# Kernel optimization log

Measured on AMD Instinct MI355X. Metric: run time of the kernel, lower is better.

Reference implementation:

```python
import jax, jax.numpy as jnp
import numpy as np
import math

Z_DIM = 1024
DOWN = 512
UP = 1024
HEADS = 16
ROPE_HD = 64
HEAD_DIM = Z_DIM // HEADS  # 64, used only in softmax scale
V_HD = UP // HEADS


def _rope(x, num_heads, head_dim, base=10000.0):
    # x: [bs, L, num_heads*head_dim] -> [bs, num_heads, L, head_dim]
    bs, L, _ = x.shape
    theta = 1.0 / (base ** (jnp.arange(0, head_dim, 2, dtype=jnp.float32) / head_dim))
    pe = jnp.arange(L, dtype=jnp.float32)[:, None] * theta[None, :]  # [L, hd/2]
    # NOTE: faithful to source, which stores sin(pos) in cos_pos and cos(pos) in sin_pos
    cos_pos = jnp.repeat(jnp.sin(pe), 2, axis=-1)  # [L, hd]
    sin_pos = jnp.repeat(jnp.cos(pe), 2, axis=-1)
    q = x.reshape(bs, L, num_heads, head_dim).transpose(0, 2, 1, 3)
    q2 = jnp.stack([-q[..., 1::2], q[..., ::2]], axis=-1).reshape(q.shape)
    return q * cos_pos + q2 * sin_pos


def setup_inputs() -> dict:
    key = jax.random.key(0)
    ks = jax.random.split(key, 20)
    B, S = 2, 2048
    s = lambda fan_in: 1.0 / math.sqrt(fan_in)
    d = {
        'query': jax.random.normal(ks[0], (B, S, Z_DIM), jnp.float32),
        'key': jax.random.normal(ks[1], (B, S, Z_DIM), jnp.float32),
        'value': jax.random.normal(ks[2], (B, S, Z_DIM), jnp.float32),
        'w_dkv': jax.random.uniform(ks[3], (Z_DIM, DOWN), jnp.float32, -s(Z_DIM), s(Z_DIM)),
        'b_dkv': jnp.zeros((DOWN,), jnp.float32),
        'w_uk': jax.random.uniform(ks[4], (DOWN, UP), jnp.float32, -s(DOWN), s(DOWN)),
        'b_uk': jnp.zeros((UP,), jnp.float32),
        'w_uv': jax.random.uniform(ks[5], (DOWN, UP), jnp.float32, -s(DOWN), s(DOWN)),
        'b_uv': jnp.zeros((UP,), jnp.float32),
        'w_dq': jax.random.uniform(ks[6], (Z_DIM, DOWN), jnp.float32, -s(Z_DIM), s(Z_DIM)),
        'b_dq': jnp.zeros((DOWN,), jnp.float32),
        'w_uq': jax.random.uniform(ks[7], (DOWN, UP), jnp.float32, -s(DOWN), s(DOWN)),
        'b_uq': jnp.zeros((UP,), jnp.float32),
        'w_qr': jax.random.uniform(ks[8], (DOWN, ROPE_HD * HEADS), jnp.float32, -s(DOWN), s(DOWN)),
        'b_qr': jnp.zeros((ROPE_HD * HEADS,), jnp.float32),
        'w_kr': jax.random.uniform(ks[9], (Z_DIM, ROPE_HD), jnp.float32, -s(Z_DIM), s(Z_DIM)),
        'b_kr': jnp.zeros((ROPE_HD,), jnp.float32),
        'w_fc': jax.random.uniform(ks[10], (HEADS * V_HD, Z_DIM), jnp.float32, -s(HEADS * V_HD), s(HEADS * V_HD)),
        'b_fc': jnp.zeros((Z_DIM,), jnp.float32),
    }
    return d


def reference(query, key, value, w_dkv, b_dkv, w_uk, b_uk, w_uv, b_uv,
              w_dq, b_dq, w_uq, b_uq, w_qr, b_qr, w_kr, b_kr, w_fc, b_fc):
    bs, S, _ = query.shape
    c_t_kv = key @ w_dkv + b_dkv                      # [B,S,down]
    k_t_c = c_t_kv @ w_uk + b_uk                      # [B,S,up]
    v_t_c = c_t_kv @ w_uv + b_uv                      # [B,S,up]
    c_t_q = query @ w_dq + b_dq                       # [B,S,down]
    q_t_c = c_t_q @ w_uq + b_uq                       # [B,S,up]
    q_t_r = _rope(c_t_q @ w_qr + b_qr, HEADS, ROPE_HD)  # [B,H,S,rope_hd]
    k_t_r = _rope(key @ w_kr + b_kr, 1, ROPE_HD)         # [B,1,S,rope_hd]

    q_t_c = q_t_c.reshape(bs, S, HEADS, V_HD).transpose(0, 2, 1, 3)  # [B,H,S,dc]
    q = jnp.concatenate([q_t_c, q_t_r], axis=-1)                      # [B,H,S,dc+dr]
    k_t_c = k_t_c.reshape(bs, S, HEADS, V_HD).transpose(0, 2, 1, 3)
    k = jnp.concatenate([k_t_c, jnp.broadcast_to(k_t_r, (bs, HEADS, S, ROPE_HD))], axis=-1)

    scores = jnp.einsum('bhqd,bhkd->bhqk', q, k)
    scale = math.sqrt(HEAD_DIM) + math.sqrt(ROPE_HD)
    attn = jax.nn.softmax(scores / scale, axis=-1)    # dropout is identity (eval / p=0)

    v = v_t_c.reshape(bs, S, HEADS, V_HD).transpose(0, 2, 1, 3)
    out = jnp.einsum('bhqk,bhkd->bhqd', attn, v)      # [B,H,S,v_hd]
    out = out.transpose(0, 2, 1, 3).reshape(bs, S, HEADS * V_HD)
    return out @ w_fc + b_fc
```

## Files before the change

### kernel.cpp

```cpp
#include <hip/hip_runtime.h>
#include <hip/hip_bf16.h>
#include <hip/hip_fp16.h>

typedef __attribute__((ext_vector_type(8))) short    bf16x8;
typedef __attribute__((ext_vector_type(4))) float    f32x4;
typedef __attribute__((ext_vector_type(4))) _Float16 f16x4;
typedef __attribute__((ext_vector_type(8))) _Float16 f16x8;
typedef __attribute__((ext_vector_type(2))) __fp16   fp16x2_raw;

typedef const void __attribute__((address_space(1))) gvoid_t;
typedef void __attribute__((address_space(3)))       lvoid_t;

static __device__ __forceinline__ void gload_lds16(const void* g, void* l) {
    __builtin_amdgcn_global_load_lds((gvoid_t*)g, (lvoid_t*)l, 16, 0, 0);
}

static __device__ __forceinline__ short bfbits(float f) {
    union { __hip_bfloat16 h; short s; } u;
    u.h = __float2bfloat16(f);
    return u.s;
}

__global__ __launch_bounds__(256) void cvt_bf16_dual(const float* __restrict__ q,
                                                     const float* __restrict__ k,
                                                     __hip_bfloat16* __restrict__ qd,
                                                     __hip_bfloat16* __restrict__ kd, int n8) {
    int t = blockIdx.x * 256 + threadIdx.x;
    const float* src;
    __hip_bfloat16* dst;
    int i;
    if (t < n8)          { src = q; dst = qd; i = t; }
    else if (t < 2 * n8) { src = k; dst = kd; i = t - n8; }
    else return;
    float4 a = ((const float4*)src)[2 * i];
    float4 b = ((const float4*)src)[2 * i + 1];
    bf16x8 o;
    o[0] = bfbits(a.x); o[1] = bfbits(a.y); o[2] = bfbits(a.z); o[3] = bfbits(a.w);
    o[4] = bfbits(b.x); o[5] = bfbits(b.y); o[6] = bfbits(b.z); o[7] = bfbits(b.w);
    ((bf16x8*)dst)[i] = o;
}

struct TJob { const float* src; __hip_bfloat16* dst; int K, N, tx; };
struct TJobPack { TJob j[8]; int start[8]; };

__global__ __launch_bounds__(256) void transpose_cvt_batch(TJobPack P) {
    __shared__ __hip_bfloat16 tile[64][72];
    const int bid = blockIdx.x;
    int ji = 0;
#pragma unroll
    for (int k = 1; k < 8; ++k) if (bid >= P.start[k]) ji = k;
    const TJob J = P.j[ji];
    const int local = bid - P.start[ji];
    const int kb = (local % J.tx) * 64;
    const int nb = (local / J.tx) * 64;
    const int c  = threadIdx.x & 63;
    const int r0 = threadIdx.x >> 6;
    if (nb < J.N) {
#pragma unroll
        for (int i = 0; i < 16; ++i) {
            int r = r0 + i * 4;
            tile[r][c] = __float2bfloat16(J.src[(size_t)(kb + r) * J.N + nb + c]);
        }
        __syncthreads();
#pragma unroll
        for (int i = 0; i < 16; ++i) {
            int r = r0 + i * 4;
            J.dst[(size_t)(nb + r) * J.K + kb + c] = tile[c][r];
        }
    } else {
        __hip_bfloat16 z = __float2bfloat16(0.0f);
#pragma unroll
        for (int i = 0; i < 16; ++i) {
            int r = r0 + i * 4;
            J.dst[(size_t)(nb + r) * J.K + kb + c] = z;
        }
    }
}

__global__ __launch_bounds__(256) void bias_prep(const float* __restrict__ b_dkv, const float* __restrict__ b_kr,
                                                 const float* __restrict__ b_uk,  const float* __restrict__ b_uv,
                                                 const float* __restrict__ b_uq,  const float* __restrict__ b_qr,
                                                 float* __restrict__ bcat1, float* __restrict__ bcat2,
                                                 float* __restrict__ bcat3) {
    int t = blockIdx.x * 256 + threadIdx.x;
    if (t < 640) {
        bcat1[t] = (t < 512) ? b_dkv[t] : ((t - 512) < 64 ? b_kr[t - 512] : 0.0f);
    } else if (t < 2688) {
        int u = t - 640;
        bcat2[u] = (u < 1024) ? b_uq[u] : b_qr[u - 1024];
    } else if (t < 4736) {
        int u = t - 2688;
        bcat3[u] = (u < 1024) ? b_uk[u] : b_uv[u - 1024];
    }
}

struct GJob {
    const __hip_bfloat16* A; const __hip_bfloat16* Bt; const float* bias;
    void* C0; void* C1; int N, K, lda, ldb, ldc; float scale; int mode;
};

__global__ __launch_bounds__(256) void gemm_dual(GJob j0, GJob j1, int split) {
    __shared__ __align__(16) __hip_bfloat16 sA[2][64 * 32];
    __shared__ __align__(16) __hip_bfloat16 sB[2][128 * 32];
    const GJob J  = (blockIdx.x < (unsigned)split) ? j0 : j1;
    const int bx  = (blockIdx.x < (unsigned)split) ? blockIdx.x : blockIdx.x - split;
    const int tid  = threadIdx.x;
    const int wid  = tid >> 6;
    const int lane = tid & 63;
    const int lr   = lane & 15;
    const int lg   = lane >> 4;
    const int mb   = blockIdx.y * 64;
    const int nb   = bx * 128;
    const int wr   = (wid >> 1) * 32;
    const int wc   = (wid & 1) * 64;

    auto stage = [&](int bufi, int k0) {
        {
            int e   = wid * 512 + lane * 8;
            int row = e >> 5, col = e & 31;
            gload_lds16(J.A + (size_t)(mb + row) * J.lda + (k0 + col), &sA[bufi][wid * 512]);
        }
#pragma unroll
        for (int j = 0; j < 2; ++j) {
            int cb  = wid * 2 + j;
            int e   = cb * 512 + lane * 8;
            int row = e >> 5, col = e & 31;
            gload_lds16(J.Bt + (size_t)(nb + row) * J.ldb + (k0 + col), &sB[bufi][cb * 512]);
        }
    };

    f32x4 acc[2][4] = {};
    const int nt = J.K / 32;
    stage(0, 0);
    asm volatile("s_waitcnt vmcnt(0)" ::: "memory");
    __syncthreads();

    for (int t = 0; t < nt; ++t) {
        const int cur = t & 1;
        if (t + 1 < nt) stage(cur ^ 1, (t + 1) * 32);
        bf16x8 af[2], bfr[4];
#pragma unroll
        for (int m = 0; m < 2; ++m)
            af[m] = *(const bf16x8*)&sA[cur][(wr + m * 16 + lr) * 32 + lg * 8];
#pragma unroll
        for (int n = 0; n < 4; ++n)
            bfr[n] = *(const bf16x8*)&sB[cur][(wc + n * 16 + lr) * 32 + lg * 8];
#pragma unroll
        for (int m = 0; m < 2; ++m)
#pragma unroll
            for (int n = 0; n < 4; ++n)
                acc[m][n] = __builtin_amdgcn_mfma_f32_16x16x32_bf16(af[m], bfr[n], acc[m][n], 0, 0, 0);
        asm volatile("s_waitcnt vmcnt(0)" ::: "memory");
        __syncthreads();
    }

#pragma unroll
    for (int n = 0; n < 4; ++n) {
        int col  = nb + wc + n * 16 + lr;
        float bv = J.bias ? J.bias[col] : 0.0f;
#pragma unroll
        for (int m = 0; m < 2; ++m) {
#pragma unroll
            for (int r = 0; r < 4; ++r) {
                int row    = mb + wr + m * 16 + lg * 4 + r;
                float val  = (acc[m][n][r] + bv) * J.scale;
                if (J.mode == 1) ((float*)J.C0)[(size_t)row * J.ldc + col] = val;
                else             ((__hip_bfloat16*)J.C0)[(size_t)row * J.ldc + col] = __float2bfloat16(val);
            }
        }
    }
}

__global__ __launch_bounds__(256) void gemm128_dual(GJob j0, GJob j1, int split, int Rtot) {
    __shared__ __align__(16) char smem[128 * 132 * 2];
    __hip_bfloat16* sA = (__hip_bfloat16*)smem;
    __hip_bfloat16* sB = (__hip_bfloat16*)(smem + 16384);
    const GJob J  = (blockIdx.x < (unsigned)split) ? j0 : j1;
    const int bx  = (blockIdx.x < (unsigned)split) ? blockIdx.x : blockIdx.x - split;
    const int tid  = threadIdx.x;
    const int wid  = tid >> 6;
    const int lane = tid & 63;
    const int lr   = lane & 15;
    const int lg   = lane >> 4;
    const int mb   = blockIdx.y * 128;
    const int nb   = bx * 128;
    const int wr   = (wid >> 1) * 64;
    const int wc   = (wid & 1) * 64;

    auto stage = [&](int bufi, int k0) {
#pragma unroll
        for (int j = 0; j < 2; ++j) {
            int c   = wid * 2 + j;
            int e   = c * 512 + lane * 8;
            int row = e >> 5, col = e & 31;
            gload_lds16(J.A + (size_t)(mb + row) * J.lda + (k0 + col), &sA[bufi * 4096 + c * 512]);
        }
#pragma unroll
        for (int j = 0; j < 2; ++j) {
            int c   = wid * 2 + j;
            int e   = c * 512 + lane * 8;
            int row = e >> 5, col = e & 31;
            gload_lds16(J.Bt + (size_t)(nb + row) * J.ldb + (k0 + col), &sB[bufi * 4096 + c * 512]);
        }
    };

    f32x4 acc[4][4] = {};
    const int nt = J.K / 32;
    stage(0, 0);
    asm volatile("s_waitcnt vmcnt(0)" ::: "memory");
    __syncthreads();

    for (int t = 0; t < nt; ++t) {
        const int cur = t & 1;
        if (t + 1 < nt) stage(cur ^ 1, (t + 1) * 32);
        bf16x8 af[4], bfr[4];
#pragma unroll
        for (int m = 0; m < 4; ++m)
            af[m] = *(const bf16x8*)&sA[cur * 4096 + (wr + m * 16 + lr) * 32 + lg * 8];
#pragma unroll
        for (int n = 0; n < 4; ++n)
            bfr[n] = *(const bf16x8*)&sB[cur * 4096 + (wc + n * 16 + lr) * 32 + lg * 8];
#pragma unroll
        for (int m = 0; m < 4; ++m)
#pragma unroll
            for (int n = 0; n < 4; ++n)
                acc[m][n] = __builtin_amdgcn_mfma_f32_16x16x32_bf16(af[m], bfr[n], acc[m][n], 0, 0, 0);
        asm volatile("s_waitcnt vmcnt(0)" ::: "memory");
        __syncthreads();
    }

    if (J.mode == 3 && nb >= 1024) {
        _Float16* T = (_Float16*)smem;
#pragma unroll
        for (int n = 0; n < 4; ++n) {
            int cl = wc + n * 16 + lr;
            float bv = J.bias[nb + cl];
#pragma unroll
            for (int m = 0; m < 4; ++m)
#pragma unroll
                for (int r = 0; r < 4; ++r)
                    T[cl * 132 + wr + m * 16 + lg * 4 + r] =
                        (_Float16)((acc[m][n][r] + bv) * J.scale);
        }
        __syncthreads();
        const int vd   = tid >> 1;
        const int half = tid & 1;
        _Float16* dst = (_Float16*)J.C1 + (size_t)(nb - 1024 + vd) * Rtot + mb + half * 64;
        const _Float16* srcT = T + vd * 132 + half * 64;
#pragma unroll
        for (int j = 0; j < 8; ++j)
            *(f16x8*)&dst[j * 8] = *(const f16x8*)&srcT[j * 8];
        return;
    }

#pragma unroll
    for (int n = 0; n < 4; ++n) {
        int col  = nb + wc + n * 16 + lr;
        float bv = J.bias ? J.bias[col] : 0.0f;
#pragma unroll
        for (int m = 0; m < 4; ++m) {
#pragma unroll
            for (int r = 0; r < 4; ++r) {
                int row    = mb + wr + m * 16 + lg * 4 + r;
                float val  = (acc[m][n][r] + bv) * J.scale;
                if (J.mode == 3) ((__hip_bfloat16*)J.C0)[(size_t)row * 1024 + col] = __float2bfloat16(val);
                else             ((__hip_bfloat16*)J.C0)[(size_t)row * J.ldc + col] = __float2bfloat16(val);
            }
        }
    }
}

__global__ __launch_bounds__(256) void rope_kernel(__hip_bfloat16* __restrict__ qrope,
                                                   __hip_bfloat16* __restrict__ krope,
                                                   int R, int S) {
    int t = blockIdx.x * 256 + threadIdx.x;
    const int nq = R * 512;
    __hip_bfloat16* x;
    int i, row, rowstride, hh;
    if (t < nq)               { i = t & 31; hh = (t >> 5) & 15; row = t >> 9; x = qrope; rowstride = 2048; }
    else if (t < nq + R * 32) { t -= nq; i = t & 31; hh = 0; row = t >> 5; x = krope; rowstride = 640; }
    else return;
    int pos = row & (S - 1);
    float theta = __expf(-0.28782313662425572f * (float)i);
    float pe = (float)pos * theta;
    float sp, cp;
    __sincosf(pe, &sp, &cp);
    size_t idx = (size_t)row * rowstride + hh * 64 + 2 * i;
    float x0 = __bfloat162float(x[idx]);
    float x1 = __bfloat162float(x[idx + 1]);
    x[idx]     = __float2bfloat16(x0 * sp - x1 * cp);
    x[idx + 1] = __float2bfloat16(x1 * sp + x0 * cp);
}

__global__ __launch_bounds__(512, 4) void attn_kernel(const __hip_bfloat16* __restrict__ qcat,
                                                      const __hip_bfloat16* __restrict__ ktc,
                                                      const __hip_bfloat16* __restrict__ kr,
                                                      const _Float16* __restrict__ vtcT,
                                                      __hip_bfloat16* __restrict__ outp,
                                                      int S, int R) {
    __shared__ __align__(16) char lds[2][24 * 1024];
    const int tid  = threadIdx.x;
    const int wid  = tid >> 6;
    const int lane = tid & 63;
    const int lr   = lane & 15;
    const int lg   = lane >> 4;

    const int NQ   = S / 128;
    const int L    = blockIdx.x;
    const int slot = L >> 3;
    const int gg   = (L & 7) + 8 * (slot / NQ);
    const int qt   = slot % NQ;
    const int h    = gg & 15;
    const int b    = gg >> 4;
    const size_t base = (size_t)b * S;
    const int qb   = qt * 128 + wid * 16;

    auto stage = [&](int bufi, int kt) {
        char* bufK = lds[bufi];
        char* bufV = lds[bufi] + 16 * 1024;
#pragma unroll
        for (int j = 0; j < 2; ++j) {
            int c   = wid * 2 + j;
            int rho = c * 4 + (lane >> 4);
            int u   = (lane & 15) ^ (rho & 15);
            const __hip_bfloat16* src = (u < 8)
                ? ktc + (base + kt + rho) * 1024 + h * 64 + u * 8
                : kr  + (base + kt + rho) * 640 + (u & 7) * 8;
            gload_lds16(src, bufK + c * 1024);
        }
        {
            int c   = wid;
            int rho = c * 8 + (lane >> 3);
            int u   = (lane & 7) ^ (rho & 7);
            gload_lds16(vtcT + (size_t)(h * 64 + rho) * R + base + kt + u * 8,
                        bufV + c * 1024);
        }
    };

    bf16x8 qf[4];
    {
        size_t row = base + qb + lr;
        const __hip_bfloat16* pq = qcat + row * 2048 + h * 64;
        qf[0] = *(const bf16x8*)(pq + lg * 8);
        qf[1] = *(const bf16x8*)(pq + 32 + lg * 8);
        qf[2] = *(const bf16x8*)(pq + 1024 + lg * 8);
        qf[3] = *(const bf16x8*)(pq + 1024 + 32 + lg * 8);
    }

    int kbase[4], vbase[4];
#pragma unroll
    for (int c = 0; c < 4; ++c)
        kbase[c] = lr * 256 + (((c * 4 + lg) ^ lr) << 4);
#pragma unroll
    for (int st = 0; st < 4; ++st)
        vbase[st] = lr * 128 + ((((st * 2 + (lg >> 1)) ^ (lr & 7)) << 4) + (lg & 1) * 8);

    f32x4 oacc[4] = {};
    float lrun = 0.0f;

    const int NT = S / 64;
    stage(0, 0);
    __syncthreads();

    for (int t = 0; t < NT; ++t) {
        const int cur = t & 1;
        if (t + 1 < NT) stage(cur ^ 1, (t + 1) * 64);

        const char* bufK = lds[cur];
        const char* bufV = lds[cur] + 16 * 1024;

        f32x4 sacc[4] = {};
        __builtin_amdgcn_s_setprio(1);
#pragma unroll
        for (int st = 0; st < 4; ++st)
#pragma unroll
            for (int c = 0; c < 4; ++c) {
                bf16x8 kf = *(const bf16x8*)(bufK + st * 4096 + kbase[c]);
                sacc[st] = __builtin_amdgcn_mfma_f32_16x16x32_bf16(kf, qf[c], sacc[st], 0, 0, 0);
            }
        __builtin_amdgcn_s_setprio(0);

        float p[4][4];
#pragma unroll
        for (int st = 0; st < 4; ++st)
#pragma unroll
            for (int r = 0; r < 4; ++r) {
                p[st][r] = __builtin_exp2f(sacc[st][r]);
                lrun += p[st][r];
            }
        __builtin_amdgcn_s_setprio(1);
#pragma unroll
        for (int st = 0; st < 4; ++st) {
            union { fp16x2_raw h2[2]; f16x4 v; } pu;
            pu.h2[0] = __builtin_amdgcn_cvt_pkrtz(p[st][0], p[st][1]);
            pu.h2[1] = __builtin_amdgcn_cvt_pkrtz(p[st][2], p[st][3]);
#pragma unroll
            for (int vt = 0; vt < 4; ++vt) {
                f16x4 vf = *(const f16x4*)(bufV + vt * 2048 + vbase[st]);
                oacc[vt] = __builtin_amdgcn_mfma_f32_16x16x16f16(vf, pu.v, oacc[vt], 0, 0, 0);
            }
        }
        __builtin_amdgcn_s_setprio(0);
        __syncthreads();
    }

    lrun += __shfl_xor(lrun, 16);
    lrun += __shfl_xor(lrun, 32);
    float inv = 1.0f / lrun;
    size_t rowoff = (base + qb + lr) << 10;
#pragma unroll
    for (int vt = 0; vt < 4; ++vt)
#pragma unroll
        for (int r = 0; r < 4; ++r)
            outp[rowoff + h * 64 + vt * 16 + lg * 4 + r] =
                __float2bfloat16(oacc[vt][r] * inv);
}

extern "C" void kernel_launch(void* const* d_in, const int* in_sizes, int n_in,
                              void* d_out, int out_size, void* d_ws, size_t ws_size,
                              hipStream_t stream) {
    const float* query = (const float*)d_in[0];
    const float* key   = (const float*)d_in[1];
    const float* w_dkv = (const float*)d_in[3];
    const float* b_dkv = (const float*)d_in[4];
    const float* w_uk  = (const float*)d_in[5];
    const float* b_uk  = (const float*)d_in[6];
    const float* w_uv  = (const float*)d_in[7];
    const float* b_uv  = (const float*)d_in[8];
    const float* w_dq  = (const float*)d_in[9];
    const float* b_dq  = (const float*)d_in[10];
    const float* w_uq  = (const float*)d_in[11];
    const float* b_uq  = (const float*)d_in[12];
    const float* w_qr  = (const float*)d_in[13];
    const float* b_qr  = (const float*)d_in[14];
    const float* w_kr  = (const float*)d_in[15];
    const float* b_kr  = (const float*)d_in[16];
    const float* w_fc  = (const float*)d_in[17];
    const float* b_fc  = (const float*)d_in[18];

    const int B = 2;
    const int R = in_sizes[0] / 1024;
    const int S = R / B;
    const float QSCALE = 1.4426950408889634f / 16.0f;

    char* ws = (char*)d_ws;
    size_t off = 0;
    auto alloc = [&](size_t bytes) -> char* {
        char* p = ws + off;
        off += (bytes + 255) & ~(size_t)255;
        return p;
    };

    __hip_bfloat16* q_bf  = (__hip_bfloat16*)alloc((size_t)R * 1024 * 2);
    __hip_bfloat16* k_bf  = (__hip_bfloat16*)alloc((size_t)R * 1024 * 2);
    __hip_bfloat16* wcat1 = (__hip_bfloat16*)alloc(640 * 1024 * 2);
    __hip_bfloat16* wdq_t = (__hip_bfloat16*)alloc(512 * 1024 * 2);
    __hip_bfloat16* wcat3 = (__hip_bfloat16*)alloc(2048 * 512 * 2);
    __hip_bfloat16* wcat2 = (__hip_bfloat16*)alloc(2048 * 512 * 2);
    __hip_bfloat16* wfc_t = (__hip_bfloat16*)alloc(1024 * 1024 * 2);
    float*          bcat1 = (float*)alloc(640 * 4);
    float*          bcat2 = (float*)alloc(2048 * 4);
    float*          bcat3 = (float*)alloc(2048 * 4);
    __hip_bfloat16* ckkr  = (__hip_bfloat16*)alloc((size_t)R * 640 * 2);
    __hip_bfloat16* c_q   = (__hip_bfloat16*)alloc((size_t)R * 512 * 2);
    __hip_bfloat16* ktc   = (__hip_bfloat16*)alloc((size_t)R * 1024 * 2);
    _Float16*       vtcT  = (_Float16*)alloc((size_t)R * 1024 * 2);
    __hip_bfloat16* qcat  = (__hip_bfloat16*)alloc((size_t)R * 2048 * 2);
    __hip_bfloat16* attn_out = q_bf;

    cvt_bf16_dual<<<dim3(2 * R * 1024 / 8 / 256), 256, 0, stream>>>(query, key, q_bf, k_bf, R * 1024 / 8);

    TJobPack P;
    P.j[0] = {w_dkv, wcat1,              1024, 512,  16};
    P.j[1] = {w_kr,  wcat1 + 512 * 1024, 1024, 64,   16};
    P.j[2] = {w_dq,  wdq_t,              1024, 512,  16};
    P.j[3] = {w_uk,  wcat3,              512,  1024, 8};
    P.j[4] = {w_uv,  wcat3 + 1024 * 512, 512,  1024, 8};
    P.j[5] = {w_uq,  wcat2,              512,  1024, 8};
    P.j[6] = {w_qr,  wcat2 + 1024 * 512, 512,  1024, 8};
    P.j[7] = {w_fc,  wfc_t,              1024, 1024, 16};
    int st = 0;
    const int counts[8] = {128, 32, 128, 128, 128, 128, 128, 256};
    for (int i = 0; i < 8; ++i) { P.start[i] = st; st += counts[i]; }
    transpose_cvt_batch<<<dim3(st), 256, 0, stream>>>(P);

    bias_prep<<<dim3(19), 256, 0, stream>>>(b_dkv, b_kr, b_uk, b_uv, b_uq, b_qr, bcat1, bcat2, bcat3);

    GJob ja0 = {k_bf, wcat1, bcat1, ckkr, nullptr, 640, 1024, 1024, 1024, 640, 1.0f, 0};
    GJob ja1 = {q_bf, wdq_t, b_dq,  c_q,  nullptr, 512, 1024, 1024, 1024, 512, 1.0f, 0};
    gemm_dual<<<dim3(9, R / 64), 256, 0, stream>>>(ja0, ja1, 5);

    GJob jb0 = {ckkr, wcat3, bcat3, ktc,  vtcT,    2048, 512, 640, 512, 1024, 1.0f,   3};
    GJob jb1 = {c_q,  wcat2, bcat2, qcat, nullptr, 2048, 512, 512, 512, 2048, QSCALE, 0};
    gemm128_dual<<<dim3(32, R / 128), 256, 0, stream>>>(jb0, jb1, 16, R);

    rope_kernel<<<dim3((R * 512 + R * 32 + 255) / 256), 256, 0, stream>>>(qcat + 1024, ckkr + 512, R, S);

    attn_kernel<<<dim3((S / 128) * 16 * B), 512, 0, stream>>>(qcat, ktc, ckkr + 512, vtcT, attn_out, S, R);

    GJob jc0 = {attn_out, wfc_t, b_fc, d_out, nullptr, 1024, 1024, 1024, 1024, 1024, 1.0f, 1};
    gemm_dual<<<dim3(8, R / 64), 256, 0, stream>>>(jc0, jc0, 8);
}
```

Before: 179.6 us.

## Fuse RoPE into GEMM epilogues, merge prep kernels, use fdot2 for softmax sum

Merges the bf16 conversion, weight transpose and bias concatenation kernels into a single prep launch. Applies the rotary embedding directly in the GEMM epilogues via lane shuffles, removing the separate rope kernel and its read-modify-write pass. Replaces the scalar softmax denominator accumulation with fp16 dot2 on the packed probabilities. This adds sincos work and shuffles to the epilogues, and the row sum now uses fp16-rounded values.

```diff
diff --git a/kernel.cpp b/kernel.cpp
--- a/kernel.cpp
+++ b/kernel.cpp
@@ -21,76 +21,84 @@
     return u.s;
 }
 
-__global__ __launch_bounds__(256) void cvt_bf16_dual(const float* __restrict__ q,
-                                                     const float* __restrict__ k,
-                                                     __hip_bfloat16* __restrict__ qd,
-                                                     __hip_bfloat16* __restrict__ kd, int n8) {
-    int t = blockIdx.x * 256 + threadIdx.x;
-    const float* src;
-    __hip_bfloat16* dst;
-    int i;
-    if (t < n8)          { src = q; dst = qd; i = t; }
-    else if (t < 2 * n8) { src = k; dst = kd; i = t - n8; }
-    else return;
-    float4 a = ((const float4*)src)[2 * i];
-    float4 b = ((const float4*)src)[2 * i + 1];
-    bf16x8 o;
-    o[0] = bfbits(a.x); o[1] = bfbits(a.y); o[2] = bfbits(a.z); o[3] = bfbits(a.w);
-    o[4] = bfbits(b.x); o[5] = bfbits(b.y); o[6] = bfbits(b.z); o[7] = bfbits(b.w);
-    ((bf16x8*)dst)[i] = o;
+static __device__ __forceinline__ float rope_val(float val, int col, int row, int Smask) {
+    float other = __shfl_xor(val, 1);
+    float theta = __expf(-0.28782313662425572f * (float)((col >> 1) & 31));
+    float sp, cp;
+    __sincosf((float)(row & Smask) * theta, &sp, &cp);
+    return (col & 1) ? fmaf(val, sp, other * cp) : fmaf(val, sp, -other * cp);
 }
 
 struct TJob { const float* src; __hip_bfloat16* dst; int K, N, tx; };
-struct TJobPack { TJob j[8]; int start[8]; };
-
-__global__ __launch_bounds__(256) void transpose_cvt_batch(TJobPack P) {
+struct PrepArgs {
+    const float* query; const float* key;
+    __hip_bfloat16* q_bf; __hip_bfloat16* k_bf; int n8; int cvtBlocks; int tBlocks;
+    TJob j[8]; int start[8];
+    const float *b_dkv, *b_kr, *b_uk, *b_uv, *b_uq, *b_qr;
+    float *bcat1, *bcat2, *bcat3;
+};
+
+__global__ __launch_bounds__(256) void prep_kernel(PrepArgs A) {
     __shared__ __hip_bfloat16 tile[64][72];
-    const int bid = blockIdx.x;
-    int ji = 0;
-#pragma unroll
-    for (int k = 1; k < 8; ++k) if (bid >= P.start[k]) ji = k;
-    const TJob J = P.j[ji];
-    const int local = bid - P.start[ji];
-    const int kb = (local % J.tx) * 64;
-    const int nb = (local / J.tx) * 64;
-    const int c  = threadIdx.x & 63;
-    const int r0 = threadIdx.x >> 6;
-    if (nb < J.N) {
-#pragma unroll
-        for (int i = 0; i < 16; ++i) {
-            int r = r0 + i * 4;
-            tile[r][c] = __float2bfloat16(J.src[(size_t)(kb + r) * J.N + nb + c]);
-        }
-        __syncthreads();
-#pragma unroll
-        for (int i = 0; i < 16; ++i) {
-            int r = r0 + i * 4;
-            J.dst[(size_t)(nb + r) * J.K + kb + c] = tile[c][r];
-        }
-    } else {
-        __hip_bfloat16 z = __float2bfloat16(0.0f);
-#pragma unroll
-        for (int i = 0; i < 16; ++i) {
-            int r = r0 + i * 4;
-            J.dst[(size_t)(nb + r) * J.K + kb + c] = z;
-        }
-    }
-}
-
-__global__ __launch_bounds__(256) void bias_prep(const float* __restrict__ b_dkv, const float* __restrict__ b_kr,
-                                                 const float* __restrict__ b_uk,  const float* __restrict__ b_uv,
-                                                 const float* __restrict__ b_uq,  const float* __restrict__ b_qr,
-                                                 float* __restrict__ bcat1, float* __restrict__ bcat2,
-                                                 float* __restrict__ bcat3) {
-    int t = blockIdx.x * 256 + threadIdx.x;
+    int bid = blockIdx.x;
+    if (bid < A.cvtBlocks) {
+        int t = bid * 256 + threadIdx.x;
+        const float* src;
+        __hip_bfloat16* dst;
+        int i;
+        if (t < A.n8) { src = A.query; dst = A.q_bf; i = t; }
+        else          { src = A.key;   dst = A.k_bf; i = t - A.n8; }
+        float4 a = ((const float4*)src)[2 * i];
+        float4 b = ((const float4*)src)[2 * i + 1];
+        bf16x8 o;
+        o[0] = bfbits(a.x); o[1] = bfbits(a.y); o[2] = bfbits(a.z); o[3] = bfbits(a.w);
+        o[4] = bfbits(b.x); o[5] = bfbits(b.y); o[6] = bfbits(b.z); o[7] = bfbits(b.w);
+        ((bf16x8*)dst)[i] = o;
+        return;
+    }
+    bid -= A.cvtBlocks;
+    if (bid < A.tBlocks) {
+        int ji = 0;
+#pragma unroll
+        for (int k = 1; k < 8; ++k) if (bid >= A.start[k]) ji = k;
+        const TJob J = A.j[ji];
+        const int local = bid - A.start[ji];
+        const int kb = (local % J.tx) * 64;
+        const int nb = (local / J.tx) * 64;
+        const int c  = threadIdx.x & 63;
+        const int r0 = threadIdx.x >> 6;
+        if (nb < J.N) {
+#pragma unroll
+            for (int i = 0; i < 16; ++i) {
+                int r = r0 + i * 4;
+                tile[r][c] = __float2bfloat16(J.src[(size_t)(kb + r) * J.N + nb + c]);
+            }
+            __syncthreads();
+#pragma unroll
+            for (int i = 0; i < 16; ++i) {
+                int r = r0 + i * 4;
+                J.dst[(size_t)(nb + r) * J.K + kb + c] = tile[c][r];
+            }
+        } else {
+            __hip_bfloat16 z = __float2bfloat16(0.0f);
+#pragma unroll
+            for (int i = 0; i < 16; ++i) {
+                int r = r0 + i * 4;
+                J.dst[(size_t)(nb + r) * J.K + kb + c] = z;
+            }
+        }
+        return;
+    }
+    bid -= A.tBlocks;
+    int t = bid * 256 + threadIdx.x;
     if (t < 640) {
-        bcat1[t] = (t < 512) ? b_dkv[t] : ((t - 512) < 64 ? b_kr[t - 512] : 0.0f);
+        A.bcat1[t] = (t < 512) ? A.b_dkv[t] : ((t - 512) < 64 ? A.b_kr[t - 512] : 0.0f);
     } else if (t < 2688) {
         int u = t - 640;
-        bcat2[u] = (u < 1024) ? b_uq[u] : b_qr[u - 1024];
+        A.bcat2[u] = (u < 1024) ? A.b_uq[u] : A.b_qr[u - 1024];
     } else if (t < 4736) {
         int u = t - 2688;
-        bcat3[u] = (u < 1024) ? b_uk[u] : b_uv[u - 1024];
+        A.bcat3[u] = (u < 1024) ? A.b_uk[u] : A.b_uv[u - 1024];
     }
 }
 
@@ -99,7 +107,7 @@
     void* C0; void* C1; int N, K, lda, ldb, ldc; float scale; int mode;
 };
 
-__global__ __launch_bounds__(256) void gemm_dual(GJob j0, GJob j1, int split) {
+__global__ __launch_bounds__(256) void gemm_dual(GJob j0, GJob j1, int split, int Smask) {
     __shared__ __align__(16) __hip_bfloat16 sA[2][64 * 32];
     __shared__ __align__(16) __hip_bfloat16 sB[2][128 * 32];
     const GJob J  = (blockIdx.x < (unsigned)split) ? j0 : j1;
@@ -158,12 +166,14 @@
     for (int n = 0; n < 4; ++n) {
         int col  = nb + wc + n * 16 + lr;
         float bv = J.bias ? J.bias[col] : 0.0f;
+        bool doRope = (J.mode == 5) && (col >= 512) && (col < 576);
 #pragma unroll
         for (int m = 0; m < 2; ++m) {
 #pragma unroll
             for (int r = 0; r < 4; ++r) {
                 int row    = mb + wr + m * 16 + lg * 4 + r;
                 float val  = (acc[m][n][r] + bv) * J.scale;
+                if (doRope) val = rope_val(val, col, row, Smask);
                 if (J.mode == 1) ((float*)J.C0)[(size_t)row * J.ldc + col] = val;
                 else             ((__hip_bfloat16*)J.C0)[(size_t)row * J.ldc + col] = __float2bfloat16(val);
             }
@@ -186,6 +196,7 @@
     const int nb   = bx * 128;
     const int wr   = (wid >> 1) * 64;
     const int wc   = (wid & 1) * 64;
+    const int Smask = (Rtot >> 1) - 1;
 
     auto stage = [&](int bufi, int k0) {
 #pragma unroll
@@ -257,39 +268,19 @@
     for (int n = 0; n < 4; ++n) {
         int col  = nb + wc + n * 16 + lr;
         float bv = J.bias ? J.bias[col] : 0.0f;
+        bool doRope = (J.mode == 4) && (col >= 1024);
 #pragma unroll
         for (int m = 0; m < 4; ++m) {
 #pragma unroll
             for (int r = 0; r < 4; ++r) {
                 int row    = mb + wr + m * 16 + lg * 4 + r;
                 float val  = (acc[m][n][r] + bv) * J.scale;
+                if (doRope) val = rope_val(val, col, row, Smask);
                 if (J.mode == 3) ((__hip_bfloat16*)J.C0)[(size_t)row * 1024 + col] = __float2bfloat16(val);
                 else             ((__hip_bfloat16*)J.C0)[(size_t)row * J.ldc + col] = __float2bfloat16(val);
             }
         }
     }
-}
-
-__global__ __launch_bounds__(256) void rope_kernel(__hip_bfloat16* __restrict__ qrope,
-                                                   __hip_bfloat16* __restrict__ krope,
-                                                   int R, int S) {
-    int t = blockIdx.x * 256 + threadIdx.x;
-    const int nq = R * 512;
-    __hip_bfloat16* x;
-    int i, row, rowstride, hh;
-    if (t < nq)               { i = t & 31; hh = (t >> 5) & 15; row = t >> 9; x = qrope; rowstride = 2048; }
-    else if (t < nq + R * 32) { t -= nq; i = t & 31; hh = 0; row = t >> 5; x = krope; rowstride = 640; }
-    else return;
-    int pos = row & (S - 1);
-    float theta = __expf(-0.28782313662425572f * (float)i);
-    float pe = (float)pos * theta;
-    float sp, cp;
-    __sincosf(pe, &sp, &cp);
-    size_t idx = (size_t)row * rowstride + hh * 64 + 2 * i;
-    float x0 = __bfloat162float(x[idx]);
-    float x1 = __bfloat162float(x[idx + 1]);
-    x[idx]     = __float2bfloat16(x0 * sp - x1 * cp);
-    x[idx + 1] = __float2bfloat16(x1 * sp + x0 * cp);
 }
 
 __global__ __launch_bounds__(512, 4) void attn_kernel(const __hip_bfloat16* __restrict__ qcat,
@@ -357,6 +348,10 @@
 
     f32x4 oacc[4] = {};
     float lrun = 0.0f;
+#if __has_builtin(__builtin_amdgcn_fdot2)
+    fp16x2_raw one2;
+    one2[0] = (__fp16)1.0f; one2[1] = (__fp16)1.0f;
+#endif
 
     const int NT = S / 64;
     stage(0, 0);
@@ -384,16 +379,20 @@
 #pragma unroll
         for (int st = 0; st < 4; ++st)
 #pragma unroll
-            for (int r = 0; r < 4; ++r) {
+            for (int r = 0; r < 4; ++r)
                 p[st][r] = __builtin_exp2f(sacc[st][r]);
-                lrun += p[st][r];
-            }
         __builtin_amdgcn_s_setprio(1);
 #pragma unroll
         for (int st = 0; st < 4; ++st) {
             union { fp16x2_raw h2[2]; f16x4 v; } pu;
             pu.h2[0] = __builtin_amdgcn_cvt_pkrtz(p[st][0], p[st][1]);
             pu.h2[1] = __builtin_amdgcn_cvt_pkrtz(p[st][2], p[st][3]);
+#if __has_builtin(__builtin_amdgcn_fdot2)
+            lrun = __builtin_amdgcn_fdot2(pu.h2[0], one2, lrun, false);
+            lrun = __builtin_amdgcn_fdot2(pu.h2[1], one2, lrun, false);
+#else
+            lrun += p[st][0] + p[st][1] + p[st][2] + p[st][3];
+#endif
 #pragma unroll
             for (int vt = 0; vt < 4; ++vt) {
                 f16x4 vf = *(const f16x4*)(bufV + vt * 2048 + vbase[st]);
@@ -468,36 +467,39 @@
     __hip_bfloat16* qcat  = (__hip_bfloat16*)alloc((size_t)R * 2048 * 2);
     __hip_bfloat16* attn_out = q_bf;
 
-    cvt_bf16_dual<<<dim3(2 * R * 1024 / 8 / 256), 256, 0, stream>>>(query, key, q_bf, k_bf, R * 1024 / 8);
-
-    TJobPack P;
-    P.j[0] = {w_dkv, wcat1,              1024, 512,  16};
-    P.j[1] = {w_kr,  wcat1 + 512 * 1024, 1024, 64,   16};
-    P.j[2] = {w_dq,  wdq_t,              1024, 512,  16};
-    P.j[3] = {w_uk,  wcat3,              512,  1024, 8};
-    P.j[4] = {w_uv,  wcat3 + 1024 * 512, 512,  1024, 8};
-    P.j[5] = {w_uq,  wcat2,              512,  1024, 8};
-    P.j[6] = {w_qr,  wcat2 + 1024 * 512, 512,  1024, 8};
-    P.j[7] = {w_fc,  wfc_t,              1024, 1024, 16};
-    int st = 0;
-    const int counts[8] = {128, 32, 128, 128, 128, 128, 128, 256};
-    for (int i = 0; i < 8; ++i) { P.start[i] = st; st += counts[i]; }
-    transpose_cvt_batch<<<dim3(st), 256, 0, stream>>>(P);
-
-    bias_prep<<<dim3(19), 256, 0, stream>>>(b_dkv, b_kr, b_uk, b_uv, b_uq, b_qr, bcat1, bcat2, bcat3);
-
-    GJob ja0 = {k_bf, wcat1, bcat1, ckkr, nullptr, 640, 1024, 1024, 1024, 640, 1.0f, 0};
+    PrepArgs PA;
+    PA.query = query; PA.key = key; PA.q_bf = q_bf; PA.k_bf = k_bf;
+    PA.n8 = R * 1024 / 8;
+    PA.cvtBlocks = 2 * PA.n8 / 256;
+    PA.j[0] = {w_dkv, wcat1,              1024, 512,  16};
+    PA.j[1] = {w_kr,  wcat1 + 512 * 1024, 1024, 64,   16};
+    PA.j[2] = {w_dq,  wdq_t,              1024, 512,  16};
+    PA.j[3] = {w_uk,  wcat3,              512,  1024, 8};
+    PA.j[4] = {w_uv,  wcat3 + 1024 * 512, 512,  1024, 8};
+    PA.j[5] = {w_uq,  wcat2,              512,  1024, 8};
+    PA.j[6] = {w_qr,  wcat2 + 1024 * 512, 512,  1024, 8};
+    PA.j[7] = {w_fc,  wfc_t,              1024, 1024, 16};
+    {
+        int st = 0;
+        const int counts[8] = {128, 32, 128, 128, 128, 128, 128, 256};
+        for (int i = 0; i < 8; ++i) { PA.start[i] = st; st += counts[i]; }
+        PA.tBlocks = st;
+    }
+    PA.b_dkv = b_dkv; PA.b_kr = b_kr; PA.b_uk = b_uk; PA.b_uv = b_uv;
+    PA.b_uq = b_uq;   PA.b_qr = b_qr;
+    PA.bcat1 = bcat1; PA.bcat2 = bcat2; PA.bcat3 = bcat3;
+    prep_kernel<<<dim3(PA.cvtBlocks + PA.tBlocks + 19), 256, 0, stream>>>(PA);
+
+    GJob ja0 = {k_bf, wcat1, bcat1, ckkr, nullptr, 640, 1024, 1024, 1024, 640, 1.0f, 5};
     GJob ja1 = {q_bf, wdq_t, b_dq,  c_q,  nullptr, 512, 1024, 1024, 1024, 512, 1.0f, 0};
-    gemm_dual<<<dim3(9, R / 64), 256, 0, stream>>>(ja0, ja1, 5);
+    gemm_dual<<<dim3(9, R / 64), 256, 0, stream>>>(ja0, ja1, 5, S - 1);
 
     GJob jb0 = {ckkr, wcat3, bcat3, ktc,  vtcT,    2048, 512, 640, 512, 1024, 1.0f,   3};
-    GJob jb1 = {c_q,  wcat2, bcat2, qcat, nullptr, 2048, 512, 512, 512, 2048, QSCALE, 0};
+    GJob jb1 = {c_q,  wcat2, bcat2, qcat, nullptr, 2048, 512, 512, 512, 2048, QSCALE, 4};
     gemm128_dual<<<dim3(32, R / 128), 256, 0, stream>>>(jb0, jb1, 16, R);
 
-    rope_kernel<<<dim3((R * 512 + R * 32 + 255) / 256), 256, 0, stream>>>(qcat + 1024, ckkr + 512, R, S);
-
     attn_kernel<<<dim3((S / 128) * 16 * B), 512, 0, stream>>>(qcat, ktc, ckkr + 512, vtcT, attn_out, S, R);
 
     GJob jc0 = {attn_out, wfc_t, b_fc, d_out, nullptr, 1024, 1024, 1024, 1024, 1024, 1.0f, 1};
-    gemm_dual<<<dim3(8, R / 64), 256, 0, stream>>>(jc0, jc0, 8);
-}
+    gemm_dual<<<dim3(8, R / 64), 256, 0, stream>>>(jc0, jc0, 8, S - 1);
+}
```

Result: no change. 178.0 us (-0.9%).
